# Performance work log

Hardware: AMD Instinct MI355X
Metric: run time of the kernel (lower is better)

## Reference

```python
import jax, jax.numpy as jnp
import numpy as np

N_HEADS = 16
ROPE_THETA = 10000.0


def _rope_cos_sin(seq_len, head_dim):
    # freqs for pairs (2i, 2i+1): [seq_len, head_dim//2]
    inv_freq = 1.0 / (ROPE_THETA ** (jnp.arange(0, head_dim, 2, dtype=jnp.float32) / head_dim))
    angles = jnp.arange(seq_len, dtype=jnp.float32)[:, None] * inv_freq[None, :]
    return jnp.cos(angles), jnp.sin(angles)


def _apply_rope(t, cos, sin):
    # t: [B, H, S, hd]; complex multiply on interleaved pairs
    tr = t.reshape(*t.shape[:-1], -1, 2)  # [B,H,S,hd//2,2]
    x0, x1 = tr[..., 0], tr[..., 1]
    r0 = x0 * cos - x1 * sin
    r1 = x0 * sin + x1 * cos
    return jnp.stack([r0, r1], axis=-1).reshape(t.shape)


def setup_inputs() -> dict:
    key = jax.random.key(0)
    ks = jax.random.split(key, 5)
    B, S, D = 2, 2048, 2048
    scale = 0.02
    return {
        "x": jax.random.normal(ks[0], (B, S, D), jnp.float32),
        "wq": jax.random.normal(ks[1], (D, D), jnp.float32) * scale,
        "wk": jax.random.normal(ks[2], (D, D), jnp.float32) * scale,
        "wv": jax.random.normal(ks[3], (D, D), jnp.float32) * scale,
        "wo": jax.random.normal(ks[4], (D, D), jnp.float32) * scale,
    }


def reference(x, wq, wk, wv, wo):
    B, S, D = x.shape
    H = N_HEADS
    hd = D // H
    # QKV projections (Linear with no bias: x @ W.T), split heads -> [B,H,S,hd]
    def proj(w):
        return jnp.einsum('bsd,ed->bse', x, w).reshape(B, S, H, hd).transpose(0, 2, 1, 3)
    q, k, v = proj(wq), proj(wk), proj(wv)
    cos, sin = _rope_cos_sin(S, hd)  # [S, hd//2] each
    cos = cos[None, None]            # [1,1,S,hd//2]
    sin = sin[None, None]
    q = _apply_rope(q, cos, sin)
    k = _apply_rope(k, cos, sin)
    # causal SDPA
    scores = jnp.einsum('bhqd,bhkd->bhqk', q, k) / jnp.sqrt(jnp.float32(hd))
    causal = jnp.tril(jnp.ones((S, S), dtype=bool))
    scores = jnp.where(causal, scores, jnp.finfo(scores.dtype).min)
    attn = jax.nn.softmax(scores, axis=-1)
    out = jnp.einsum('bhqk,bhkd->bhqd', attn, v)
    out = out.transpose(0, 2, 1, 3).reshape(B, S, D)
    return jnp.einsum('bsd,ed->bse', out, wo)
```

## Files before the change

kernel.cpp:

```cpp
#include <hip/hip_runtime.h>
#include <stdint.h>

typedef __attribute__((ext_vector_type(4))) float f32x4;
typedef __attribute__((ext_vector_type(8))) short short8;
typedef __attribute__((ext_vector_type(4))) short s16x4;

#define DEV __device__ __forceinline__

constexpr int Bc = 2, Sc = 2048, Dc = 2048, Hc = 16, HDc = 128;
constexpr int Mc = Bc * Sc;
constexpr float ATTN_SCALE = 0.08838834764831843f;

DEV short f2bf(float f) {
  unsigned u = __float_as_uint(f);
  unsigned r = (u + 0x7fffu + ((u >> 16) & 1u)) >> 16;
  return (short)(unsigned short)r;
}

DEV void gload_lds16(const void* gsrc, void* ldst) {
  typedef const __attribute__((address_space(1))) void as1_cvoid;
  typedef __attribute__((address_space(3))) void as3_void;
  __builtin_amdgcn_global_load_lds((as1_cvoid*)(uintptr_t)gsrc,
                                   (as3_void*)(uint32_t)(uintptr_t)ldst,
                                   16, 0, 0);
}

__global__ void cast_f32_bf16(const float* __restrict__ in, short* __restrict__ out, int n8) {
  int i = blockIdx.x * 256 + threadIdx.x;
  if (i >= n8) return;
  f32x4 a = ((const f32x4*)in)[i * 2];
  f32x4 b = ((const f32x4*)in)[i * 2 + 1];
  short8 o;
  o[0] = f2bf(a[0]); o[1] = f2bf(a[1]); o[2] = f2bf(a[2]); o[3] = f2bf(a[3]);
  o[4] = f2bf(b[0]); o[5] = f2bf(b[1]); o[6] = f2bf(b[2]); o[7] = f2bf(b[3]);
  ((short8*)out)[i] = o;
}

__global__ void rope_table(float* __restrict__ ct, float* __restrict__ st) {
  int t = blockIdx.x * 256 + threadIdx.x;
  int s = t >> 6, i = t & 63;
  float freq = powf(10000.0f, -(float)(2 * i) * (1.0f / 128.0f));
  float a = (float)s * freq;
  float sv, cv;
  sincosf(a, &sv, &cv);
  ct[t] = cv; st[t] = sv;
}

template <int EPI>
__global__ __launch_bounds__(512, 2) void gemm_pipe(
    const short* __restrict__ A,
    const short* __restrict__ W0, const short* __restrict__ W1, const short* __restrict__ W2,
    short* __restrict__ qo, short* __restrict__ ko, short* __restrict__ vo,
    float* __restrict__ outf,
    const float* __restrict__ ct, const float* __restrict__ st) {
  constexpr int K = Dc, NT = K / 64;
  __shared__ short As[2][128][64];
  __shared__ short Bs[2][2][128][64];

  const int tid = threadIdx.x, lane = tid & 63, w = tid >> 6;
  const int g = lane >> 4, c = lane & 15;
  const int wr = w >> 2, wc = w & 3;

  const int nx = gridDim.x;
  const int nwg = nx * gridDim.y;
  const int flat = blockIdx.y * nx + blockIdx.x;
  const int swz = (flat & 7) * (nwg >> 3) + (flat >> 3);
  const int nbx = swz % nx, nby = swz / nx;

  const int m0 = nby * 128;
  const int which = (EPI == 0) ? (nbx >> 3) : 0;
  const int wn0 = (EPI == 0) ? ((nbx & 7) * 256) : (nbx * 256);
  const short* W = (EPI == 1) ? W0 : ((which == 0) ? W0 : (which == 1) ? W1 : W2);

  const int r1 = tid >> 3, p1 = tid & 7;
  const int psw = (p1 ^ (r1 & 7)) * 8;
  const short* gA0 = A + (size_t)(m0 + r1) * K + psw;
  const short* gA1 = gA0 + (size_t)64 * K;
  const short* gB0 = W + (size_t)(wn0 + r1) * K + psw;
  const short* gB1 = gB0 + (size_t)64 * K;
  const short* gB2 = gB0 + (size_t)128 * K;
  const short* gB3 = gB0 + (size_t)192 * K;
  char* ldsA = (char*)As + w * 1024;
  char* ldsB = (char*)Bs + w * 1024;

#define STAGE(t, db)                                        \
  do {                                                      \
    const size_t ko_ = (size_t)(t) * 64;                    \
    gload_lds16(gA0 + ko_, ldsA + (db) * 16384);            \
    gload_lds16(gA1 + ko_, ldsA + (db) * 16384 + 8192);     \
    gload_lds16(gB0 + ko_, ldsB + (db) * 32768);            \
    gload_lds16(gB1 + ko_, ldsB + (db) * 32768 + 8192);     \
    gload_lds16(gB2 + ko_, ldsB + (db) * 32768 + 16384);    \
    gload_lds16(gB3 + ko_, ldsB + (db) * 32768 + 24576);    \
  } while (0)

  f32x4 acc[4][4] = {};
  const int cx = (g ^ (c & 7)) * 16;
  const char* aBase = (const char*)As + (wr * 64 + c) * 128;
  const char* bBase = (const char*)Bs + (wc >> 1) * 16384 + ((wc & 1) * 64 + c) * 128;

  short8 afA[2][4], bfA[2][4], afB[2][4], bfB[2][4];

#define READ_FRAGS(af, bf, db)                                                        \
  do {                                                                                \
    const char* aB = aBase + (db) * 16384;                                            \
    const char* bB = bBase + (db) * 32768;                                            \
    _Pragma("unroll")                                                                 \
    for (int kk = 0; kk < 2; ++kk) {                                                  \
      const int co = cx ^ (kk * 64);                                                  \
      _Pragma("unroll")                                                               \
      for (int mi = 0; mi < 4; ++mi) af[kk][mi] = *(const short8*)(aB + mi * 2048 + co); \
      _Pragma("unroll")                                                               \
      for (int nj = 0; nj < 4; ++nj) bf[kk][nj] = *(const short8*)(bB + nj * 2048 + co); \
    }                                                                                 \
  } while (0)

#define MFMA_ALL(af, bf)                                                              \
  do {                                                                                \
    _Pragma("unroll")                                                                 \
    for (int kk = 0; kk < 2; ++kk)                                                    \
      _Pragma("unroll")                                                               \
      for (int mi = 0; mi < 4; ++mi)                                                  \
        _Pragma("unroll")                                                             \
        for (int nj = 0; nj < 4; ++nj)                                                \
          acc[mi][nj] = __builtin_amdgcn_mfma_f32_16x16x32_bf16(af[kk][mi], bf[kk][nj], acc[mi][nj], 0, 0, 0); \
  } while (0)

  STAGE(0, 0);
  STAGE(1, 1);
  asm volatile("s_waitcnt vmcnt(6)" ::: "memory");
  __builtin_amdgcn_sched_barrier(0);
  __builtin_amdgcn_s_barrier();
  READ_FRAGS(afA, bfA, 0);
  asm volatile("s_waitcnt lgkmcnt(0)" ::: "memory");
  __builtin_amdgcn_sched_barrier(0);
  __builtin_amdgcn_s_barrier();

  for (int t = 0; t < NT; t += 2) {
    if (t + 2 < NT) { STAGE(t + 2, 0); asm volatile("s_waitcnt vmcnt(6)" ::: "memory"); }
    else            { asm volatile("s_waitcnt vmcnt(0)" ::: "memory"); }
    __builtin_amdgcn_sched_barrier(0);
    __builtin_amdgcn_s_barrier();
    READ_FRAGS(afB, bfB, 1);
    __builtin_amdgcn_sched_barrier(0);
    __builtin_amdgcn_s_setprio(1);
    MFMA_ALL(afA, bfA);
    __builtin_amdgcn_s_setprio(0);
    asm volatile("s_waitcnt lgkmcnt(0)" ::: "memory");
    __builtin_amdgcn_sched_barrier(0);
    __builtin_amdgcn_s_barrier();

    if (t + 3 < NT) { STAGE(t + 3, 1); asm volatile("s_waitcnt vmcnt(6)" ::: "memory"); }
    else            { asm volatile("s_waitcnt vmcnt(0)" ::: "memory"); }
    __builtin_amdgcn_sched_barrier(0);
    __builtin_amdgcn_s_barrier();
    if (t + 2 < NT) READ_FRAGS(afA, bfA, 0);
    __builtin_amdgcn_sched_barrier(0);
    __builtin_amdgcn_s_setprio(1);
    MFMA_ALL(afB, bfB);
    __builtin_amdgcn_s_setprio(0);
    asm volatile("s_waitcnt lgkmcnt(0)" ::: "memory");
    __builtin_amdgcn_sched_barrier(0);
    __builtin_amdgcn_s_barrier();
  }
#undef STAGE
#undef READ_FRAGS
#undef MFMA_ALL

  if constexpr (EPI == 0) {
    if (which < 2) {
      short* outb = (which == 0) ? qo : ko;
#pragma unroll
      for (int mi = 0; mi < 4; ++mi)
#pragma unroll
        for (int nj = 0; nj < 4; ++nj)
#pragma unroll
          for (int r = 0; r < 4; ++r) {
            int row = m0 + wr * 64 + mi * 16 + g * 4 + r;
            int col = wn0 + wc * 64 + nj * 16 + c;
            float v = acc[mi][nj][r];
            float other = __shfl_xor(v, 1);
            int pi = (col & (HDc - 1)) >> 1;
            int sp = row & (Sc - 1);
            float cv = ct[sp * 64 + pi], sv = st[sp * 64 + pi];
            v = ((col & 1) == 0) ? (v * cv - other * sv) : (other * sv + v * cv);
            int b_ = row >> 11, sq = row & (Sc - 1);
            int h_ = col >> 7, dd = col & (HDc - 1);
            outb[((size_t)(b_ * Hc + h_) * Sc + sq) * HDc + dd] = f2bf(v);
          }
    } else {
#pragma unroll
      for (int mi = 0; mi < 4; ++mi)
#pragma unroll
        for (int nj = 0; nj < 4; ++nj) {
          int row0 = m0 + wr * 64 + mi * 16 + g * 4;
          int col = wn0 + wc * 64 + nj * 16 + c;
          int b_ = row0 >> 11, sq0 = row0 & (Sc - 1);
          int h_ = col >> 7, dd = col & (HDc - 1);
          s16x4 pk;
#pragma unroll
          for (int r = 0; r < 4; ++r) pk[r] = f2bf(acc[mi][nj][r]);
          *(s16x4*)&vo[((size_t)(b_ * Hc + h_) * HDc + dd) * Sc + sq0] = pk;
        }
    }
  } else {
#pragma unroll
    for (int mi = 0; mi < 4; ++mi)
#pragma unroll
      for (int nj = 0; nj < 4; ++nj)
#pragma unroll
        for (int r = 0; r < 4; ++r) {
          int row = m0 + wr * 64 + mi * 16 + g * 4 + r;
          int col = wn0 + wc * 64 + nj * 16 + c;
          outf[(size_t)row * Dc + col] = acc[mi][nj][r];
        }
  }
}

DEV void stage_kv(const short* kh, const short* vth, int kv0,
                  short* Kb, short* Vb, int w, int tid) {
#pragma unroll
  for (int i = 0; i < 4; ++i) {
    int L = i * 256 + tid;
    int row = L >> 4, p = L & 15;
    gload_lds16(kh + (size_t)(kv0 + row) * HDc + ((p ^ (row & 7)) * 8),
                (char*)Kb + i * 4096 + w * 1024);
  }
#pragma unroll
  for (int i = 0; i < 4; ++i) {
    int L = i * 256 + tid;
    int row = L >> 3, p = L & 7;
    gload_lds16(vth + (size_t)row * Sc + kv0 + ((p ^ (row & 7)) * 8),
                (char*)Vb + i * 4096 + w * 1024);
  }
}

__global__ __launch_bounds__(256) void attn_kernel(
    const short* __restrict__ qb, const short* __restrict__ kb,
    const short* __restrict__ vtb, short* __restrict__ ob) {
  __shared__ short Kl[2][64 * 128];
  __shared__ short Vl[2][128 * 64];
  __shared__ short Pl[4 * 16 * 72];

  const int tid = threadIdx.x, lane = tid & 63, w = tid >> 6;
  const int g = lane >> 4, c = lane & 15;
  const int bh = blockIdx.y;
  const int b_ = bh >> 4, h_ = bh & 15;
  const short* qh = qb + (size_t)bh * Sc * HDc;
  const short* kh = kb + (size_t)bh * Sc * HDc;
  const short* vth = vtb + (size_t)bh * HDc * Sc;

  for (int pass = 0; pass < 2; ++pass) {
    const int qt = pass ? (31 - blockIdx.x) : blockIdx.x;
    const int q0 = qt * 64;

    short8 qf[4];
#pragma unroll
    for (int kc = 0; kc < 4; ++kc)
      qf[kc] = *(const short8*)&qh[(size_t)(q0 + w * 16 + c) * HDc + kc * 32 + g * 8];

    float mrow[4], lrow[4];
    f32x4 acc[8] = {};
#pragma unroll
    for (int r = 0; r < 4; ++r) { mrow[r] = -1e30f; lrow[r] = 0.f; }

    const int nt = qt + 1;
    int cur = 0;
    stage_kv(kh, vth, 0, Kl[0], Vl[0], w, tid);
    __syncthreads();

    for (int kvt = 0; kvt < nt; ++kvt) {
      if (kvt + 1 < nt)
        stage_kv(kh, vth, (kvt + 1) * 64, Kl[cur ^ 1], Vl[cur ^ 1], w, tid);

      f32x4 sacc[4];
#pragma unroll
      for (int kb_ = 0; kb_ < 4; ++kb_) {
        sacc[kb_] = (f32x4){0.f, 0.f, 0.f, 0.f};
#pragma unroll
        for (int kc = 0; kc < 4; ++kc) {
          short8 kf = *(const short8*)&Kl[cur][(kb_ * 16 + c) * 128 + (((kc * 4 + g) ^ (c & 7)) * 8)];
          sacc[kb_] = __builtin_amdgcn_mfma_f32_16x16x32_bf16(qf[kc], kf, sacc[kb_], 0, 0, 0);
        }
      }
      float p[4][4];
      const bool last = (kvt == qt);
      const int kv0 = kvt * 64;
#pragma unroll
      for (int kb_ = 0; kb_ < 4; ++kb_)
#pragma unroll
        for (int r = 0; r < 4; ++r) {
          float s = sacc[kb_][r] * ATTN_SCALE;
          if (last) {
            int qg = q0 + w * 16 + g * 4 + r;
            int kg = kv0 + kb_ * 16 + c;
            if (kg > qg) s = -1e30f;
          }
          p[kb_][r] = s;
        }
      float scal[4];
#pragma unroll
      for (int r = 0; r < 4; ++r) {
        float v = fmaxf(fmaxf(p[0][r], p[1][r]), fmaxf(p[2][r], p[3][r]));
        v = fmaxf(v, __shfl_xor(v, 1));
        v = fmaxf(v, __shfl_xor(v, 2));
        v = fmaxf(v, __shfl_xor(v, 4));
        v = fmaxf(v, __shfl_xor(v, 8));
        float mn = fmaxf(mrow[r], v);
        scal[r] = __expf(mrow[r] - mn);
        mrow[r] = mn;
      }
#pragma unroll
      for (int r = 0; r < 4; ++r) {
        float acc_s = 0.f;
#pragma unroll
        for (int kb_ = 0; kb_ < 4; ++kb_) {
          p[kb_][r] = __expf(p[kb_][r] - mrow[r]);
          acc_s += p[kb_][r];
        }
        acc_s += __shfl_xor(acc_s, 1);
        acc_s += __shfl_xor(acc_s, 2);
        acc_s += __shfl_xor(acc_s, 4);
        acc_s += __shfl_xor(acc_s, 8);
        lrow[r] = lrow[r] * scal[r] + acc_s;
      }
#pragma unroll
      for (int db = 0; db < 8; ++db)
#pragma unroll
        for (int r = 0; r < 4; ++r) acc[db][r] *= scal[r];
#pragma unroll
      for (int kb_ = 0; kb_ < 4; ++kb_)
#pragma unroll
        for (int r = 0; r < 4; ++r)
          Pl[w * 16 * 72 + (g * 4 + r) * 72 + kb_ * 16 + c] = f2bf(p[kb_][r]);
      short8 pa[2];
#pragma unroll
      for (int k2 = 0; k2 < 2; ++k2)
        pa[k2] = *(const short8*)&Pl[w * 16 * 72 + c * 72 + k2 * 32 + g * 8];
#pragma unroll
      for (int db = 0; db < 8; ++db)
#pragma unroll
        for (int k2 = 0; k2 < 2; ++k2) {
          short8 vf = *(const short8*)&Vl[cur][(db * 16 + c) * 64 + (((k2 * 4 + g) ^ (c & 7)) * 8)];
          acc[db] = __builtin_amdgcn_mfma_f32_16x16x32_bf16(pa[k2], vf, acc[db], 0, 0, 0);
        }
      __syncthreads();
      cur ^= 1;
    }

#pragma unroll
    for (int db = 0; db < 8; ++db)
#pragma unroll
      for (int r = 0; r < 4; ++r) {
        int qg = q0 + w * 16 + g * 4 + r;
        int d = db * 16 + c;
        float v = acc[db][r] / lrow[r];
        ob[((size_t)(b_ * Sc + qg)) * Dc + h_ * HDc + d] = f2bf(v);
      }
  }
}

extern "C" void kernel_launch(void* const* d_in, const int* in_sizes, int n_in,
                              void* d_out, int out_size, void* d_ws, size_t ws_size,
                              hipStream_t stream) {
  const float* x = (const float*)d_in[0];
  const float* wq = (const float*)d_in[1];
  const float* wk = (const float*)d_in[2];
  const float* wv = (const float*)d_in[3];
  const float* wo = (const float*)d_in[4];
  float* out = (float*)d_out;

  char* ws = (char*)d_ws;
  short* xb  = (short*)(ws + 0);
  short* wqb = (short*)(ws + 16777216);
  short* wkb = (short*)(ws + 25165824);
  short* wvb = (short*)(ws + 33554432);
  short* wob = (short*)(ws + 41943040);
  short* qb  = (short*)(ws + 50331648);
  short* kbf = (short*)(ws + 67108864);
  short* vtb = (short*)(ws + 83886080);
  float* ct  = (float*)(ws + 100663296);
  float* st  = (float*)(ws + 101187584);
  short* obuf = xb;

  cast_f32_bf16<<<Mc * Dc / 8 / 256, 256, 0, stream>>>(x, xb, Mc * Dc / 8);
  cast_f32_bf16<<<Dc * Dc / 8 / 256, 256, 0, stream>>>(wq, wqb, Dc * Dc / 8);
  cast_f32_bf16<<<Dc * Dc / 8 / 256, 256, 0, stream>>>(wk, wkb, Dc * Dc / 8);
  cast_f32_bf16<<<Dc * Dc / 8 / 256, 256, 0, stream>>>(wv, wvb, Dc * Dc / 8);
  cast_f32_bf16<<<Dc * Dc / 8 / 256, 256, 0, stream>>>(wo, wob, Dc * Dc / 8);
  rope_table<<<Sc * 64 / 256, 256, 0, stream>>>(ct, st);

  gemm_pipe<0><<<dim3(24, 32), 512, 0, stream>>>(xb, wqb, wkb, wvb, qb, kbf, vtb, nullptr, ct, st);

  attn_kernel<<<dim3(Sc / 128, Bc * Hc), 256, 0, stream>>>(qb, kbf, vtb, obuf);

  gemm_pipe<1><<<dim3(8, 32), 512, 0, stream>>>(obuf, wob, nullptr, nullptr,
                                                nullptr, nullptr, nullptr, out, ct, st);
}
```

Measured before the change: 392.4 us.

## Use 256x256 tiles with 4-stage half-K pipeline for fused QKV GEMM

Replaces the templated QKV GEMM with a dedicated kernel that computes 256x256 output tiles per workgroup. Each wave now holds 8x4 accumulators, and K is staged in 32-wide half-slices across four LDS buffers with interleaved loads and MFMA phases. The larger tile raises arithmetic intensity and halves the A/B global traffic per output element. The cost is more register pressure and a grid of 384 workgroups, which may fill the CUs less evenly. The output projection GEMM is split into its own non-templated kernel with unchanged behaviour.

```diff
diff --git a/kernel.cpp b/kernel.cpp
--- a/kernel.cpp
+++ b/kernel.cpp
@@ -46,13 +46,169 @@
   ct[t] = cv; st[t] = sv;
 }
 
-template <int EPI>
-__global__ __launch_bounds__(512, 2) void gemm_pipe(
+__global__ __launch_bounds__(512, 2) void gemm8_qkv(
     const short* __restrict__ A,
-    const short* __restrict__ W0, const short* __restrict__ W1, const short* __restrict__ W2,
-    short* __restrict__ qo, short* __restrict__ ko, short* __restrict__ vo,
-    float* __restrict__ outf,
+    const short* __restrict__ Wq, const short* __restrict__ Wk, const short* __restrict__ Wv,
+    short* __restrict__ qo, short* __restrict__ ko_, short* __restrict__ vo,
     const float* __restrict__ ct, const float* __restrict__ st) {
+  constexpr int K = Dc, NT = K / 64;
+  __shared__ short As[4][8192];
+  __shared__ short Bs[4][8192];
+
+  const int tid = threadIdx.x, lane = tid & 63, w = tid >> 6;
+  const int g = lane >> 4, c = lane & 15;
+  const int wr = w >> 2, wc = w & 3;
+
+  const int nx = gridDim.x;
+  const int nwg = nx * gridDim.y;
+  const int flat = blockIdx.y * nx + blockIdx.x;
+  const int swz = (flat & 7) * (nwg >> 3) + (flat >> 3);
+  const int bx = swz % nx, by = swz / nx;
+
+  const int m0 = by * 256;
+  const int which = bx >> 3;
+  const int n0 = (bx & 7) * 256;
+  const short* Wm = (which == 0) ? Wq : (which == 1) ? Wk : Wv;
+
+  const short* gA = A  + (size_t)(m0 + (tid >> 2)) * K + (tid & 3) * 8;
+  const short* gB = Wm + (size_t)(n0 + (tid >> 2)) * K + (tid & 3) * 8;
+  char* aW = (char*)As + w * 1024;
+  char* bW = (char*)Bs + w * 1024;
+  const char* aR = (const char*)As + (wr * 128 + c) * 64 + g * 16;
+  const char* bR = (const char*)Bs + (wc * 64 + c) * 64 + g * 16;
+
+#define STG8(ptr, dst, koff)                                        \
+  do {                                                              \
+    gload_lds16((ptr) + (koff), (dst));                             \
+    gload_lds16((ptr) + (size_t)128 * K + (koff), (dst) + 8192);    \
+  } while (0)
+
+  f32x4 acc[8][4] = {};
+  short8 Af[4], Bf[4];
+
+  STG8(gA, aW + 0 * 16384, 0);
+  STG8(gB, bW + 0 * 16384, 0);
+  STG8(gA, aW + 1 * 16384, 32);
+  STG8(gB, bW + 1 * 16384, 32);
+  STG8(gA, aW + 2 * 16384, 64);
+  STG8(gB, bW + 2 * 16384, 64);
+  STG8(gA, aW + 3 * 16384, 96);
+  STG8(gB, bW + 3 * 16384, 96);
+  asm volatile("s_waitcnt vmcnt(8)" ::: "memory");
+  __builtin_amdgcn_sched_barrier(0);
+  __builtin_amdgcn_s_barrier();
+  __builtin_amdgcn_sched_barrier(0);
+
+#define RDA(base)                                   \
+  Af[0] = *(const short8*)((base));                 \
+  Af[1] = *(const short8*)((base) + 1024);          \
+  Af[2] = *(const short8*)((base) + 2048);          \
+  Af[3] = *(const short8*)((base) + 3072)
+#define RDB(base)                                   \
+  Bf[0] = *(const short8*)((base));                 \
+  Bf[1] = *(const short8*)((base) + 1024);          \
+  Bf[2] = *(const short8*)((base) + 2048);          \
+  Bf[3] = *(const short8*)((base) + 3072)
+#define MM(mb)                                      \
+  _Pragma("unroll")                                 \
+  for (int mi = 0; mi < 4; ++mi)                    \
+    _Pragma("unroll")                               \
+    for (int nj = 0; nj < 4; ++nj)                  \
+      acc[(mb) + mi][nj] = __builtin_amdgcn_mfma_f32_16x16x32_bf16(Af[mi], Bf[nj], acc[(mb) + mi][nj], 0, 0, 0)
+#define SYNC_PRE()                                   \
+  __builtin_amdgcn_s_barrier();                      \
+  asm volatile("s_waitcnt lgkmcnt(0)" ::: "memory"); \
+  __builtin_amdgcn_sched_barrier(0)
+#define SYNC_POST()                                  \
+  __builtin_amdgcn_s_barrier();                      \
+  __builtin_amdgcn_sched_barrier(0)
+
+  for (int t = 0; t < NT; ++t) {
+    const int so = (t & 1) * 32768;
+    RDB(bR + so);
+    RDA(aR + so);
+    if (t >= 1 && t + 1 < NT) STG8(gA, aW + (((t + 1) & 1) * 2 + 1) * 16384, (size_t)(t + 1) * 64 + 32);
+    SYNC_PRE();
+    __builtin_amdgcn_s_setprio(1);
+    MM(0);
+    __builtin_amdgcn_s_setprio(0);
+    SYNC_POST();
+    RDA(aR + so + 4096);
+    if (t + 2 < NT) STG8(gB, bW + ((t & 1) * 2) * 16384, (size_t)(t + 2) * 64);
+    SYNC_PRE();
+    __builtin_amdgcn_s_setprio(1);
+    MM(4);
+    __builtin_amdgcn_s_setprio(0);
+    SYNC_POST();
+    RDB(bR + so + 16384);
+    RDA(aR + so + 16384);
+    if (t + 2 < NT) STG8(gA, aW + ((t & 1) * 2) * 16384, (size_t)(t + 2) * 64);
+    SYNC_PRE();
+    __builtin_amdgcn_s_setprio(1);
+    MM(0);
+    __builtin_amdgcn_s_setprio(0);
+    SYNC_POST();
+    RDA(aR + so + 16384 + 4096);
+    if (t + 2 < NT) {
+      STG8(gB, bW + ((t & 1) * 2 + 1) * 16384, (size_t)(t + 2) * 64 + 32);
+      asm volatile("s_waitcnt vmcnt(6)" ::: "memory");
+    } else {
+      asm volatile("s_waitcnt vmcnt(0)" ::: "memory");
+    }
+    __builtin_amdgcn_sched_barrier(0);
+    SYNC_PRE();
+    __builtin_amdgcn_s_setprio(1);
+    MM(4);
+    __builtin_amdgcn_s_setprio(0);
+    SYNC_POST();
+  }
+#undef STG8
+#undef RDA
+#undef RDB
+#undef MM
+#undef SYNC_PRE
+#undef SYNC_POST
+
+  if (which < 2) {
+    short* outb = (which == 0) ? qo : ko_;
+#pragma unroll
+    for (int mi8 = 0; mi8 < 8; ++mi8)
+#pragma unroll
+      for (int nj = 0; nj < 4; ++nj)
+#pragma unroll
+        for (int r = 0; r < 4; ++r) {
+          int row = m0 + wr * 128 + mi8 * 16 + g * 4 + r;
+          int col = n0 + wc * 64 + nj * 16 + c;
+          float v = acc[mi8][nj][r];
+          float other = __shfl_xor(v, 1);
+          int pi = (col & (HDc - 1)) >> 1;
+          int sp = row & (Sc - 1);
+          float cv = ct[sp * 64 + pi], sv = st[sp * 64 + pi];
+          v = ((col & 1) == 0) ? (v * cv - other * sv) : (other * sv + v * cv);
+          int b_ = row >> 11, sq = row & (Sc - 1);
+          int h_ = col >> 7, dd = col & (HDc - 1);
+          outb[((size_t)(b_ * Hc + h_) * Sc + sq) * HDc + dd] = f2bf(v);
+        }
+  } else {
+#pragma unroll
+    for (int mi8 = 0; mi8 < 8; ++mi8)
+#pragma unroll
+      for (int nj = 0; nj < 4; ++nj) {
+        int row0 = m0 + wr * 128 + mi8 * 16 + g * 4;
+        int col = n0 + wc * 64 + nj * 16 + c;
+        int b_ = row0 >> 11, sq0 = row0 & (Sc - 1);
+        int h_ = col >> 7, dd = col & (HDc - 1);
+        s16x4 pk;
+#pragma unroll
+        for (int r = 0; r < 4; ++r) pk[r] = f2bf(acc[mi8][nj][r]);
+        *(s16x4*)&vo[((size_t)(b_ * Hc + h_) * HDc + dd) * Sc + sq0] = pk;
+      }
+  }
+}
+
+__global__ __launch_bounds__(512, 2) void gemm_pipe_out(
+    const short* __restrict__ A, const short* __restrict__ W0,
+    float* __restrict__ outf) {
   constexpr int K = Dc, NT = K / 64;
   __shared__ short As[2][128][64];
   __shared__ short Bs[2][2][128][64];
@@ -68,15 +224,13 @@
   const int nbx = swz % nx, nby = swz / nx;
 
   const int m0 = nby * 128;
-  const int which = (EPI == 0) ? (nbx >> 3) : 0;
-  const int wn0 = (EPI == 0) ? ((nbx & 7) * 256) : (nbx * 256);
-  const short* W = (EPI == 1) ? W0 : ((which == 0) ? W0 : (which == 1) ? W1 : W2);
+  const int wn0 = nbx * 256;
 
   const int r1 = tid >> 3, p1 = tid & 7;
   const int psw = (p1 ^ (r1 & 7)) * 8;
   const short* gA0 = A + (size_t)(m0 + r1) * K + psw;
   const short* gA1 = gA0 + (size_t)64 * K;
-  const short* gB0 = W + (size_t)(wn0 + r1) * K + psw;
+  const short* gB0 = W0 + (size_t)(wn0 + r1) * K + psw;
   const short* gB1 = gB0 + (size_t)64 * K;
   const short* gB2 = gB0 + (size_t)128 * K;
   const short* gB3 = gB0 + (size_t)192 * K;
@@ -167,54 +321,16 @@
 #undef READ_FRAGS
 #undef MFMA_ALL
 
-  if constexpr (EPI == 0) {
-    if (which < 2) {
-      short* outb = (which == 0) ? qo : ko;
-#pragma unroll
-      for (int mi = 0; mi < 4; ++mi)
-#pragma unroll
-        for (int nj = 0; nj < 4; ++nj)
-#pragma unroll
-          for (int r = 0; r < 4; ++r) {
-            int row = m0 + wr * 64 + mi * 16 + g * 4 + r;
-            int col = wn0 + wc * 64 + nj * 16 + c;
-            float v = acc[mi][nj][r];
-            float other = __shfl_xor(v, 1);
-            int pi = (col & (HDc - 1)) >> 1;
-            int sp = row & (Sc - 1);
-            float cv = ct[sp * 64 + pi], sv = st[sp * 64 + pi];
-            v = ((col & 1) == 0) ? (v * cv - other * sv) : (other * sv + v * cv);
-            int b_ = row >> 11, sq = row & (Sc - 1);
-            int h_ = col >> 7, dd = col & (HDc - 1);
-            outb[((size_t)(b_ * Hc + h_) * Sc + sq) * HDc + dd] = f2bf(v);
-          }
-    } else {
-#pragma unroll
-      for (int mi = 0; mi < 4; ++mi)
-#pragma unroll
-        for (int nj = 0; nj < 4; ++nj) {
-          int row0 = m0 + wr * 64 + mi * 16 + g * 4;
-          int col = wn0 + wc * 64 + nj * 16 + c;
-          int b_ = row0 >> 11, sq0 = row0 & (Sc - 1);
-          int h_ = col >> 7, dd = col & (HDc - 1);
-          s16x4 pk;
-#pragma unroll
-          for (int r = 0; r < 4; ++r) pk[r] = f2bf(acc[mi][nj][r]);
-          *(s16x4*)&vo[((size_t)(b_ * Hc + h_) * HDc + dd) * Sc + sq0] = pk;
-        }
-    }
-  } else {
-#pragma unroll
-    for (int mi = 0; mi < 4; ++mi)
-#pragma unroll
-      for (int nj = 0; nj < 4; ++nj)
-#pragma unroll
-        for (int r = 0; r < 4; ++r) {
-          int row = m0 + wr * 64 + mi * 16 + g * 4 + r;
-          int col = wn0 + wc * 64 + nj * 16 + c;
-          outf[(size_t)row * Dc + col] = acc[mi][nj][r];
-        }
-  }
+#pragma unroll
+  for (int mi = 0; mi < 4; ++mi)
+#pragma unroll
+    for (int nj = 0; nj < 4; ++nj)
+#pragma unroll
+      for (int r = 0; r < 4; ++r) {
+        int row = m0 + wr * 64 + mi * 16 + g * 4 + r;
+        int col = wn0 + wc * 64 + nj * 16 + c;
+        outf[(size_t)row * Dc + col] = acc[mi][nj][r];
+      }
 }
 
 DEV void stage_kv(const short* kh, const short* vth, int kv0,
@@ -390,10 +506,9 @@
   cast_f32_bf16<<<Dc * Dc / 8 / 256, 256, 0, stream>>>(wo, wob, Dc * Dc / 8);
   rope_table<<<Sc * 64 / 256, 256, 0, stream>>>(ct, st);
 
-  gemm_pipe<0><<<dim3(24, 32), 512, 0, stream>>>(xb, wqb, wkb, wvb, qb, kbf, vtb, nullptr, ct, st);
+  gemm8_qkv<<<dim3(24, 16), 512, 0, stream>>>(xb, wqb, wkb, wvb, qb, kbf, vtb, ct, st);
 
   attn_kernel<<<dim3(Sc / 128, Bc * Hc), 256, 0, stream>>>(qb, kbf, vtb, obuf);
 
-  gemm_pipe<1><<<dim3(8, 32), 512, 0, stream>>>(obuf, wob, nullptr, nullptr,
-                                                nullptr, nullptr, nullptr, out, ct, st);
-}
+  gemm_pipe_out<<<dim3(8, 32), 512, 0, stream>>>(obuf, wob, out);
+}
```

Result: slower. 410.0 us (+4.5%).
